# Optimization experiments

Measured on AMD Instinct MI355X. Metric: run time of the kernel, lower is better.

## Reference

```python
import jax, jax.numpy as jnp
import numpy as np

N_NODES = 50000
N_EDGES = 800000
IN_DIM = 128
OUT_DIM = 64


def setup_inputs() -> dict:
    key = jax.random.key(0)
    k1, k2, k3, k4 = jax.random.split(key, 4)
    x = jax.random.normal(k1, (N_NODES, IN_DIM), dtype=jnp.float32)
    edge_index = jax.random.randint(k2, (2, N_EDGES), 0, N_NODES, dtype=jnp.int64)
    # learned params: W: Linear(in_dim, out_dim, bias=False); att: Linear(2*out_dim, 1, bias=False)
    W = jax.random.normal(k3, (IN_DIM, OUT_DIM), dtype=jnp.float32) * 0.05
    att = jax.random.normal(k4, (2 * OUT_DIM, 1), dtype=jnp.float32) * 0.05
    return {"x": x, "edge_index": edge_index, "W": W, "att": att}


def reference(x, edge_index, W, att):
    n = x.shape[0]
    h = x @ W  # [N, D]
    src, dst = edge_index[0], edge_index[1]
    # per-edge attention logit: leaky_relu(att^T [h_src ; h_dst])
    e = jnp.concatenate([h[src], h[dst]], axis=-1) @ att  # [E, 1]
    e = jax.nn.leaky_relu(e[:, 0], negative_slope=0.2)  # [E]
    # segment softmax over edges grouped by destination node
    m = jax.ops.segment_max(e, dst, num_segments=n)  # [N]
    ex = jnp.exp(e - m[dst])  # [E]
    denom = jax.ops.segment_sum(ex, dst, num_segments=n)  # [N]
    alpha = ex / denom[dst]  # [E]
    # weighted scatter-add aggregation
    agg = jax.ops.segment_sum(alpha[:, None] * h[src], dst, num_segments=n)  # [N, D]
    return jax.nn.elu(agg)
```

## Files before the change

### kernel.cpp

```cpp
#include <hip/hip_runtime.h>
#include <hip/hip_bf16.h>
#include <hip/hip_fp16.h>
#include <math.h>

#define N_NODES 50000
#define N_EDGES 800000
#define IN_DIM 128
#define OUT_DIM 64

typedef __attribute__((ext_vector_type(8))) short bf16x8;
typedef __attribute__((ext_vector_type(4))) float f32x4;

static __device__ __forceinline__ ushort f2bf(float f) {
  uint u = __float_as_uint(f);
  uint r = (u + 0x7fffu + ((u >> 16) & 1u)) >> 16;
  return (ushort)r;
}
static __device__ __forceinline__ float bf2f(ushort h) {
  return __uint_as_float(((uint)h) << 16);
}

#define N4 (N_NODES / 4)
#define SCAN_NB ((N4 + 255) / 256)
#define GEMM_NB ((N_NODES + 63) / 64)
#define E4 (N_EDGES / 4)
#define K4_T (N_EDGES / 8)

__global__ __launch_bounds__(256) void k0_zero(int* __restrict__ deg) {
  int i4 = blockIdx.x * 256 + threadIdx.x;
  if (i4 < N4) ((int4*)deg)[i4] = make_int4(0, 0, 0, 0);
}

__global__ __launch_bounds__(256) void k12_fused(
    const float* __restrict__ x, const float* __restrict__ W,
    const float* __restrict__ att, const int* __restrict__ dstp,
    __half* __restrict__ h, float* __restrict__ a1, float* __restrict__ a2,
    int* __restrict__ deg, int* __restrict__ rank) {
  __shared__ __align__(16) ushort Ah[64 * 128];
  __shared__ __align__(16) ushort Al[64 * 128];
  __shared__ __align__(16) ushort Bh[64 * 128];

  int tid = threadIdx.x;
  int row0 = blockIdx.x * 64;

  int e4 = blockIdx.x * 256 + tid;
  bool has_e = e4 < E4;
  int4 d4 = make_int4(0, 0, 0, 0);
  if (has_e) d4 = ((const int4*)dstp)[e4];

#pragma unroll
  for (int it = 0; it < 8; ++it) {
    int i4 = it * 256 + tid;
    int row = i4 >> 5;
    int kq = i4 & 31;
    int grow = row0 + row;
    if (grow > N_NODES - 1) grow = N_NODES - 1;
    float4 v = ((const float4*)x)[(size_t)grow * 32 + kq];
    ushort4 hi, lo;
    hi.x = f2bf(v.x); lo.x = f2bf(v.x - bf2f(hi.x));
    hi.y = f2bf(v.y); lo.y = f2bf(v.y - bf2f(hi.y));
    hi.z = f2bf(v.z); lo.z = f2bf(v.z - bf2f(hi.z));
    hi.w = f2bf(v.w); lo.w = f2bf(v.w - bf2f(hi.w));
    int idx = (row * 128 + kq * 4) ^ ((row & 7) << 3);
    *(ushort4*)&Ah[idx] = hi;
    *(ushort4*)&Al[idx] = lo;
  }

  {
    int c = tid & 63, kq = tid >> 6;
#pragma unroll
    for (int jj = 0; jj < 4; ++jj) {
      int kb = kq * 32 + jj * 8;
      uint4 ph;
      uint hp[8];
#pragma unroll
      for (int q = 0; q < 8; ++q) hp[q] = f2bf(W[(size_t)(kb + q) * OUT_DIM + c]);
      ph.x = hp[0] | (hp[1] << 16); ph.y = hp[2] | (hp[3] << 16);
      ph.z = hp[4] | (hp[5] << 16); ph.w = hp[6] | (hp[7] << 16);
      int idx = (c * 128 + kb) ^ ((c & 7) << 3);
      *(uint4*)&Bh[idx] = ph;
    }
  }
  __syncthreads();

  int w = tid >> 6, l = tid & 63;
  int ml = l & 15, kg = l >> 4;

  f32x4 acc[4];
#pragma unroll
  for (int nt = 0; nt < 4; ++nt) acc[nt] = (f32x4){0.f, 0.f, 0.f, 0.f};

#pragma unroll
  for (int ks = 0; ks < 4; ++ks) {
    int arow = w * 16 + ml;
    int aidx = (arow * 128 + ks * 32 + kg * 8) ^ ((arow & 7) << 3);
    bf16x8 a_h = *(const bf16x8*)&Ah[aidx];
    bf16x8 a_l = *(const bf16x8*)&Al[aidx];
#pragma unroll
    for (int nt = 0; nt < 4; ++nt) {
      int brow = nt * 16 + ml;
      int bidx = (brow * 128 + ks * 32 + kg * 8) ^ ((brow & 7) << 3);
      bf16x8 b_h = *(const bf16x8*)&Bh[bidx];
      acc[nt] = __builtin_amdgcn_mfma_f32_16x16x32_bf16(a_h, b_h, acc[nt], 0, 0, 0);
      acc[nt] = __builtin_amdgcn_mfma_f32_16x16x32_bf16(a_l, b_h, acc[nt], 0, 0, 0);
    }
  }

  float t1[4], t2[4];
#pragma unroll
  for (int nt = 0; nt < 4; ++nt) {
    t1[nt] = att[nt * 16 + ml];
    t2[nt] = att[OUT_DIM + nt * 16 + ml];
  }
#pragma unroll
  for (int r = 0; r < 4; ++r) {
    int drow = kg * 4 + r;
    int grow = row0 + w * 16 + drow;
    bool ok = grow < N_NODES;
    float p1 = 0.f, p2 = 0.f;
#pragma unroll
    for (int nt = 0; nt < 4; ++nt) {
      float d = acc[nt][r];
      if (ok) h[(size_t)grow * OUT_DIM + nt * 16 + ml] = __float2half(d);
      p1 = fmaf(d, t1[nt], p1);
      p2 = fmaf(d, t2[nt], p2);
    }
#pragma unroll
    for (int o = 1; o <= 8; o <<= 1) {
      p1 += __shfl_xor(p1, o, 64);
      p2 += __shfl_xor(p2, o, 64);
    }
    if (ml == 0 && ok) { a1[grow] = p1; a2[grow] = p2; }
  }

  if (has_e) {
    int4 r4;
    r4.x = atomicAdd(&deg[d4.x], 1);
    r4.y = atomicAdd(&deg[d4.y], 1);
    r4.z = atomicAdd(&deg[d4.z], 1);
    r4.w = atomicAdd(&deg[d4.w], 1);
    ((int4*)rank)[e4] = r4;
  }
}

__global__ __launch_bounds__(256) void k3a_scan(const int* __restrict__ deg,
                                                int* __restrict__ off,
                                                int* __restrict__ bsum) {
  __shared__ int sw[4];
  int tid = threadIdx.x, lane = tid & 63, wid = tid >> 6;
  int i4 = blockIdx.x * 256 + tid;
  int4 v = make_int4(0, 0, 0, 0);
  if (i4 < N4) v = ((const int4*)deg)[i4];
  int local = v.x + v.y + v.z + v.w;
  int incl = local;
#pragma unroll
  for (int o = 1; o < 64; o <<= 1) {
    int t = __shfl_up(incl, o, 64);
    if (lane >= o) incl += t;
  }
  if (lane == 63) sw[wid] = incl;
  __syncthreads();
  if (tid == 0) {
    int c = 0;
#pragma unroll
    for (int ww = 0; ww < 4; ++ww) { int t = sw[ww]; sw[ww] = c; c += t; }
    bsum[blockIdx.x] = c;
  }
  __syncthreads();
  int excl = incl - local + sw[wid];
  int4 o;
  o.x = excl; o.y = o.x + v.x; o.z = o.y + v.y; o.w = o.z + v.z;
  if (i4 < N4) ((int4*)off)[i4] = o;
}

__global__ __launch_bounds__(256) void k3c_add(int* __restrict__ off,
                                               const int* __restrict__ bsum,
                                               const float* __restrict__ a2,
                                               int2* __restrict__ oa2) {
  __shared__ int sb[64];
  int tid = threadIdx.x;
  if (tid < 64) {
    int v = (tid < SCAN_NB) ? bsum[tid] : 0;
    int incl = v;
#pragma unroll
    for (int o = 1; o < 64; o <<= 1) {
      int t = __shfl_up(incl, o, 64);
      if (tid >= o) incl += t;
    }
    sb[tid] = incl - v;
  }
  __syncthreads();
  int i4 = blockIdx.x * 256 + tid;
  if (i4 == 0) off[N_NODES] = N_EDGES;
  if (i4 >= N4) return;
  int add = sb[blockIdx.x];
  int4 v = ((const int4*)off)[i4];
  v.x += add; v.y += add; v.z += add; v.w += add;
  ((int4*)off)[i4] = v;
  float4 a = ((const float4*)a2)[i4];
  int4 p0 = make_int4(v.x, __float_as_int(a.x), v.y, __float_as_int(a.y));
  int4 p1 = make_int4(v.z, __float_as_int(a.z), v.w, __float_as_int(a.w));
  ((int4*)oa2)[i4 * 2] = p0;
  ((int4*)oa2)[i4 * 2 + 1] = p1;
}

__global__ __launch_bounds__(256) void k4_scatter(
    const int* __restrict__ src, const int* __restrict__ dstp,
    const int* __restrict__ rank,
    const float* __restrict__ a1, const int2* __restrict__ oa2,
    int2* __restrict__ sedge) {
  int t = blockIdx.x * 256 + threadIdx.x;
  if (t >= K4_T) return;
  int4 s0 = ((const int4*)src)[t * 2],  s1 = ((const int4*)src)[t * 2 + 1];
  int4 d0 = ((const int4*)dstp)[t * 2], d1 = ((const int4*)dstp)[t * 2 + 1];
  int4 r0 = ((const int4*)rank)[t * 2], r1 = ((const int4*)rank)[t * 2 + 1];
  float A[8];
  A[0] = a1[s0.x]; A[1] = a1[s0.y]; A[2] = a1[s0.z]; A[3] = a1[s0.w];
  A[4] = a1[s1.x]; A[5] = a1[s1.y]; A[6] = a1[s1.z]; A[7] = a1[s1.w];
  int2 O[8];
  O[0] = oa2[d0.x]; O[1] = oa2[d0.y]; O[2] = oa2[d0.z]; O[3] = oa2[d0.w];
  O[4] = oa2[d1.x]; O[5] = oa2[d1.y]; O[6] = oa2[d1.z]; O[7] = oa2[d1.w];
  int S[8] = {s0.x, s0.y, s0.z, s0.w, s1.x, s1.y, s1.z, s1.w};
  int R[8] = {r0.x, r0.y, r0.z, r0.w, r1.x, r1.y, r1.z, r1.w};
#pragma unroll
  for (int q = 0; q < 8; ++q) {
    float e = A[q] + __int_as_float(O[q].y);
    e = e > 0.f ? e : 0.2f * e;
    sedge[O[q].x + R[q]] = make_int2(S[q], __float_as_int(__expf(e)));
  }
}

__global__ __launch_bounds__(256) void k5_agg(
    const int* __restrict__ off, const int2* __restrict__ sedge,
    const __half* __restrict__ h, float* __restrict__ out) {
  int tid = threadIdx.x;
  int g = tid >> 3, gl = tid & 7;
  int n = blockIdx.x * 32 + g;
  if (n >= N_NODES) return;
  int b = off[n], e = off[n + 1];

  float sum = 0.f;
  float a0 = 0.f, a1_ = 0.f, a2_ = 0.f, a3 = 0.f;
  float a4 = 0.f, a5 = 0.f, a6 = 0.f, a7 = 0.f;
  const __half* __restrict__ hb = h;

#define K5_ACC(rr, ww)                                                        \
  {                                                                           \
    float2 f;                                                                 \
    f = __half22float2(__builtin_bit_cast(__half2, rr.x));                    \
    a0 = fmaf(ww, f.x, a0); a1_ = fmaf(ww, f.y, a1_);                         \
    f = __half22float2(__builtin_bit_cast(__half2, rr.y));                    \
    a2_ = fmaf(ww, f.x, a2_); a3 = fmaf(ww, f.y, a3);                         \
    f = __half22float2(__builtin_bit_cast(__half2, rr.z));                    \
    a4 = fmaf(ww, f.x, a4); a5 = fmaf(ww, f.y, a5);                           \
    f = __half22float2(__builtin_bit_cast(__half2, rr.w));                    \
    a6 = fmaf(ww, f.x, a6); a7 = fmaf(ww, f.y, a7);                           \
  }

  int j = b;
  for (; j + 7 < e; j += 8) {
    int2 s0 = sedge[j + 0], s1 = sedge[j + 1], s2 = sedge[j + 2], s3 = sedge[j + 3];
    int2 s4 = sedge[j + 4], s5 = sedge[j + 5], s6 = sedge[j + 6], s7 = sedge[j + 7];
    uint4 r0 = ((const uint4*)(hb + (size_t)s0.x * OUT_DIM))[gl];
    uint4 r1 = ((const uint4*)(hb + (size_t)s1.x * OUT_DIM))[gl];
    uint4 r2 = ((const uint4*)(hb + (size_t)s2.x * OUT_DIM))[gl];
    uint4 r3 = ((const uint4*)(hb + (size_t)s3.x * OUT_DIM))[gl];
    uint4 r4 = ((const uint4*)(hb + (size_t)s4.x * OUT_DIM))[gl];
    uint4 r5 = ((const uint4*)(hb + (size_t)s5.x * OUT_DIM))[gl];
    uint4 r6 = ((const uint4*)(hb + (size_t)s6.x * OUT_DIM))[gl];
    uint4 r7 = ((const uint4*)(hb + (size_t)s7.x * OUT_DIM))[gl];
    float w0 = __int_as_float(s0.y), w1 = __int_as_float(s1.y);
    float w2 = __int_as_float(s2.y), w3 = __int_as_float(s3.y);
    float w4 = __int_as_float(s4.y), w5 = __int_as_float(s5.y);
    float w6 = __int_as_float(s6.y), w7 = __int_as_float(s7.y);
    sum += ((w0 + w1) + (w2 + w3)) + ((w4 + w5) + (w6 + w7));
    K5_ACC(r0, w0); K5_ACC(r1, w1); K5_ACC(r2, w2); K5_ACC(r3, w3);
    K5_ACC(r4, w4); K5_ACC(r5, w5); K5_ACC(r6, w6); K5_ACC(r7, w7);
  }
  for (; j + 3 < e; j += 4) {
    int2 s0 = sedge[j + 0], s1 = sedge[j + 1], s2 = sedge[j + 2], s3 = sedge[j + 3];
    uint4 r0 = ((const uint4*)(hb + (size_t)s0.x * OUT_DIM))[gl];
    uint4 r1 = ((const uint4*)(hb + (size_t)s1.x * OUT_DIM))[gl];
    uint4 r2 = ((const uint4*)(hb + (size_t)s2.x * OUT_DIM))[gl];
    uint4 r3 = ((const uint4*)(hb + (size_t)s3.x * OUT_DIM))[gl];
    float w0 = __int_as_float(s0.y), w1 = __int_as_float(s1.y);
    float w2 = __int_as_float(s2.y), w3 = __int_as_float(s3.y);
    sum += (w0 + w1) + (w2 + w3);
    K5_ACC(r0, w0); K5_ACC(r1, w1); K5_ACC(r2, w2); K5_ACC(r3, w3);
  }
  for (; j < e; ++j) {
    int2 s0 = sedge[j];
    uint4 r0 = ((const uint4*)(hb + (size_t)s0.x * OUT_DIM))[gl];
    float w0 = __int_as_float(s0.y);
    sum += w0;
    K5_ACC(r0, w0);
  }

  float inv = (e > b) ? 1.f / sum : 0.f;
  a0 *= inv; a1_ *= inv; a2_ *= inv; a3 *= inv;
  a4 *= inv; a5 *= inv; a6 *= inv; a7 *= inv;
  float4 o0, o1;
  o0.x = a0 > 0.f ? a0 : (__expf(a0) - 1.f);
  o0.y = a1_ > 0.f ? a1_ : (__expf(a1_) - 1.f);
  o0.z = a2_ > 0.f ? a2_ : (__expf(a2_) - 1.f);
  o0.w = a3 > 0.f ? a3 : (__expf(a3) - 1.f);
  o1.x = a4 > 0.f ? a4 : (__expf(a4) - 1.f);
  o1.y = a5 > 0.f ? a5 : (__expf(a5) - 1.f);
  o1.z = a6 > 0.f ? a6 : (__expf(a6) - 1.f);
  o1.w = a7 > 0.f ? a7 : (__expf(a7) - 1.f);
  float4* ob = (float4*)(out + (size_t)n * OUT_DIM);
  ob[gl * 2] = o0;
  ob[gl * 2 + 1] = o1;
}

extern "C" void kernel_launch(void* const* d_in, const int* in_sizes, int n_in,
                              void* d_out, int out_size, void* d_ws, size_t ws_size,
                              hipStream_t stream) {
  const float* x   = (const float*)d_in[0];
  const int*   ei  = (const int*)d_in[1];
  const float* W   = (const float*)d_in[2];
  const float* att = (const float*)d_in[3];
  float* out = (float*)d_out;

  char* p = (char*)d_ws;
  __half* h  = (__half*)p;  p += (size_t)N_NODES * OUT_DIM * sizeof(__half);
  float* a1  = (float*)p;   p += (size_t)N_NODES * sizeof(float);
  float* a2  = (float*)p;   p += (size_t)N_NODES * sizeof(float);
  int*   deg = (int*)p;     p += (size_t)N_NODES * sizeof(int);
  int*   off = (int*)p;     p += (size_t)(N_NODES + 4) * sizeof(int);
  int2*  oa2 = (int2*)p;    p += (size_t)N_NODES * sizeof(int2);
  int*   rank = (int*)p;    p += (size_t)N_EDGES * sizeof(int);
  int2*  sedge = (int2*)p;  p += (size_t)N_EDGES * sizeof(int2);
  int*   bsum = (int*)p;    p += 64 * sizeof(int);

  const int* src  = ei;
  const int* dstp = ei + N_EDGES;

  k0_zero<<<SCAN_NB, 256, 0, stream>>>(deg);
  k12_fused<<<GEMM_NB, 256, 0, stream>>>(x, W, att, dstp, h, a1, a2, deg, rank);
  k3a_scan<<<SCAN_NB, 256, 0, stream>>>(deg, off, bsum);
  k3c_add<<<SCAN_NB, 256, 0, stream>>>(off, bsum, a2, oa2);
  k4_scatter<<<(K4_T + 255) / 256, 256, 0, stream>>>(src, dstp, rank, a1, oa2, sedge);
  k5_agg<<<(N_NODES + 31) / 32, 256, 0, stream>>>(off, sedge, h, out);
}
```

Measured before the change: 107.2 us.

## Split fused GEMM/degree kernel, pre-transpose W to bf16, load operands directly to registers

```diff
diff --git a/kernel.cpp b/kernel.cpp
--- a/kernel.cpp
+++ b/kernel.cpp
@@ -23,68 +23,59 @@
 #define N4 (N_NODES / 4)
 #define SCAN_NB ((N4 + 255) / 256)
 #define GEMM_NB ((N_NODES + 63) / 64)
-#define E4 (N_EDGES / 4)
+#define K2_T (N_EDGES / 8)
 #define K4_T (N_EDGES / 8)
 
-__global__ __launch_bounds__(256) void k0_zero(int* __restrict__ deg) {
-  int i4 = blockIdx.x * 256 + threadIdx.x;
-  if (i4 < N4) ((int4*)deg)[i4] = make_int4(0, 0, 0, 0);
-}
-
-__global__ __launch_bounds__(256) void k12_fused(
-    const float* __restrict__ x, const float* __restrict__ W,
-    const float* __restrict__ att, const int* __restrict__ dstp,
-    __half* __restrict__ h, float* __restrict__ a1, float* __restrict__ a2,
-    int* __restrict__ deg, int* __restrict__ rank) {
-  __shared__ __align__(16) ushort Ah[64 * 128];
-  __shared__ __align__(16) ushort Al[64 * 128];
-  __shared__ __align__(16) ushort Bh[64 * 128];
-
+__global__ __launch_bounds__(256) void k0_prep(const float* __restrict__ W,
+                                               int* __restrict__ deg,
+                                               ushort* __restrict__ WTbf) {
+  int t = blockIdx.x * 256 + threadIdx.x;
+  if (t < N4) ((int4*)deg)[t] = make_int4(0, 0, 0, 0);
+  if (t < IN_DIM * OUT_DIM) {
+    int k = t >> 6, c = t & 63;
+    WTbf[c * IN_DIM + k] = f2bf(W[t]);
+  }
+}
+
+__global__ __launch_bounds__(256) void k1_mfma(
+    const float* __restrict__ x, const ushort* __restrict__ WTbf,
+    const float* __restrict__ att,
+    __half* __restrict__ h, float* __restrict__ a1, float* __restrict__ a2) {
   int tid = threadIdx.x;
-  int row0 = blockIdx.x * 64;
-
-  int e4 = blockIdx.x * 256 + tid;
-  bool has_e = e4 < E4;
-  int4 d4 = make_int4(0, 0, 0, 0);
-  if (has_e) d4 = ((const int4*)dstp)[e4];
-
-#pragma unroll
-  for (int it = 0; it < 8; ++it) {
-    int i4 = it * 256 + tid;
-    int row = i4 >> 5;
-    int kq = i4 & 31;
-    int grow = row0 + row;
-    if (grow > N_NODES - 1) grow = N_NODES - 1;
-    float4 v = ((const float4*)x)[(size_t)grow * 32 + kq];
-    ushort4 hi, lo;
-    hi.x = f2bf(v.x); lo.x = f2bf(v.x - bf2f(hi.x));
-    hi.y = f2bf(v.y); lo.y = f2bf(v.y - bf2f(hi.y));
-    hi.z = f2bf(v.z); lo.z = f2bf(v.z - bf2f(hi.z));
-    hi.w = f2bf(v.w); lo.w = f2bf(v.w - bf2f(hi.w));
-    int idx = (row * 128 + kq * 4) ^ ((row & 7) << 3);
-    *(ushort4*)&Ah[idx] = hi;
-    *(ushort4*)&Al[idx] = lo;
-  }
-
-  {
-    int c = tid & 63, kq = tid >> 6;
-#pragma unroll
-    for (int jj = 0; jj < 4; ++jj) {
-      int kb = kq * 32 + jj * 8;
-      uint4 ph;
-      uint hp[8];
-#pragma unroll
-      for (int q = 0; q < 8; ++q) hp[q] = f2bf(W[(size_t)(kb + q) * OUT_DIM + c]);
-      ph.x = hp[0] | (hp[1] << 16); ph.y = hp[2] | (hp[3] << 16);
-      ph.z = hp[4] | (hp[5] << 16); ph.w = hp[6] | (hp[7] << 16);
-      int idx = (c * 128 + kb) ^ ((c & 7) << 3);
-      *(uint4*)&Bh[idx] = ph;
-    }
-  }
-  __syncthreads();
-
   int w = tid >> 6, l = tid & 63;
   int ml = l & 15, kg = l >> 4;
+  int row0 = blockIdx.x * 64;
+
+  int arow = row0 + w * 16 + ml;
+  if (arow > N_NODES - 1) arow = N_NODES - 1;
+  const float* __restrict__ xr = x + (size_t)arow * IN_DIM + kg * 8;
+
+  bf16x8 b[4][4];
+#pragma unroll
+  for (int nt = 0; nt < 4; ++nt) {
+    const ushort* wc = WTbf + (nt * 16 + ml) * IN_DIM + kg * 8;
+#pragma unroll
+    for (int ks = 0; ks < 4; ++ks)
+      b[nt][ks] = *(const bf16x8*)(wc + ks * 32);
+  }
+
+  bf16x8 a_h[4], a_l[4];
+#pragma unroll
+  for (int ks = 0; ks < 4; ++ks) {
+    float4 v0 = *(const float4*)(xr + ks * 32);
+    float4 v1 = *(const float4*)(xr + ks * 32 + 4);
+    float vv[8] = {v0.x, v0.y, v0.z, v0.w, v1.x, v1.y, v1.z, v1.w};
+    ushort hh[8], ll[8];
+#pragma unroll
+    for (int q = 0; q < 8; ++q) {
+      hh[q] = f2bf(vv[q]);
+      ll[q] = f2bf(vv[q] - bf2f(hh[q]));
+    }
+    a_h[ks] = (bf16x8){(short)hh[0], (short)hh[1], (short)hh[2], (short)hh[3],
+                       (short)hh[4], (short)hh[5], (short)hh[6], (short)hh[7]};
+    a_l[ks] = (bf16x8){(short)ll[0], (short)ll[1], (short)ll[2], (short)ll[3],
+                       (short)ll[4], (short)ll[5], (short)ll[6], (short)ll[7]};
+  }
 
   f32x4 acc[4];
 #pragma unroll
@@ -92,17 +83,10 @@
 
 #pragma unroll
   for (int ks = 0; ks < 4; ++ks) {
-    int arow = w * 16 + ml;
-    int aidx = (arow * 128 + ks * 32 + kg * 8) ^ ((arow & 7) << 3);
-    bf16x8 a_h = *(const bf16x8*)&Ah[aidx];
-    bf16x8 a_l = *(const bf16x8*)&Al[aidx];
 #pragma unroll
     for (int nt = 0; nt < 4; ++nt) {
-      int brow = nt * 16 + ml;
-      int bidx = (brow * 128 + ks * 32 + kg * 8) ^ ((brow & 7) << 3);
-      bf16x8 b_h = *(const bf16x8*)&Bh[bidx];
-      acc[nt] = __builtin_amdgcn_mfma_f32_16x16x32_bf16(a_h, b_h, acc[nt], 0, 0, 0);
-      acc[nt] = __builtin_amdgcn_mfma_f32_16x16x32_bf16(a_l, b_h, acc[nt], 0, 0, 0);
+      acc[nt] = __builtin_amdgcn_mfma_f32_16x16x32_bf16(a_h[ks], b[nt][ks], acc[nt], 0, 0, 0);
+      acc[nt] = __builtin_amdgcn_mfma_f32_16x16x32_bf16(a_l[ks], b[nt][ks], acc[nt], 0, 0, 0);
     }
   }
 
@@ -132,15 +116,26 @@
     }
     if (ml == 0 && ok) { a1[grow] = p1; a2[grow] = p2; }
   }
-
-  if (has_e) {
-    int4 r4;
-    r4.x = atomicAdd(&deg[d4.x], 1);
-    r4.y = atomicAdd(&deg[d4.y], 1);
-    r4.z = atomicAdd(&deg[d4.z], 1);
-    r4.w = atomicAdd(&deg[d4.w], 1);
-    ((int4*)rank)[e4] = r4;
-  }
+}
+
+__global__ __launch_bounds__(256) void k2_rank(const int* __restrict__ dstp,
+                                               int* __restrict__ deg,
+                                               int* __restrict__ rank) {
+  int t = blockIdx.x * 256 + threadIdx.x;
+  if (t >= K2_T) return;
+  int4 d0 = ((const int4*)dstp)[t * 2];
+  int4 d1 = ((const int4*)dstp)[t * 2 + 1];
+  int4 r0, r1;
+  r0.x = atomicAdd(&deg[d0.x], 1);
+  r0.y = atomicAdd(&deg[d0.y], 1);
+  r0.z = atomicAdd(&deg[d0.z], 1);
+  r0.w = atomicAdd(&deg[d0.w], 1);
+  r1.x = atomicAdd(&deg[d1.x], 1);
+  r1.y = atomicAdd(&deg[d1.y], 1);
+  r1.z = atomicAdd(&deg[d1.z], 1);
+  r1.w = atomicAdd(&deg[d1.w], 1);
+  ((int4*)rank)[t * 2] = r0;
+  ((int4*)rank)[t * 2 + 1] = r1;
 }
 
 __global__ __launch_bounds__(256) void k3a_scan(const int* __restrict__ deg,
@@ -332,12 +327,14 @@
   int*   rank = (int*)p;    p += (size_t)N_EDGES * sizeof(int);
   int2*  sedge = (int2*)p;  p += (size_t)N_EDGES * sizeof(int2);
   int*   bsum = (int*)p;    p += 64 * sizeof(int);
+  ushort* WTbf = (ushort*)p; p += (size_t)OUT_DIM * IN_DIM * sizeof(ushort);
 
   const int* src  = ei;
   const int* dstp = ei + N_EDGES;
 
-  k0_zero<<<SCAN_NB, 256, 0, stream>>>(deg);
-  k12_fused<<<GEMM_NB, 256, 0, stream>>>(x, W, att, dstp, h, a1, a2, deg, rank);
+  k0_prep<<<SCAN_NB, 256, 0, stream>>>(W, deg, WTbf);
+  k2_rank<<<(K2_T + 255) / 256, 256, 0, stream>>>(dstp, deg, rank);
+  k1_mfma<<<GEMM_NB, 256, 0, stream>>>(x, WTbf, att, h, a1, a2);
   k3a_scan<<<SCAN_NB, 256, 0, stream>>>(deg, off, bsum);
   k3c_add<<<SCAN_NB, 256, 0, stream>>>(off, bsum, a2, oa2);
   k4_scatter<<<(K4_T + 255) / 256, 256, 0, stream>>>(src, dstp, rank, a1, oa2, sedge);
```

Result: faster. 103.6 us (-3.4%).
